# Optimization experiments

Measured on AMD Instinct MI355X. Metric: run time of the kernel, lower is better.

## Reference

```python
import jax, jax.numpy as jnp
import numpy as np

B, N, F_IN, H, C = 64, 512, 128, 128, 10
RATIO, NEG_SLOPE, LAMB = 0.5, 0.2, 1.0
K1 = int(np.ceil(RATIO * N))    # 256 nodes kept after pool1
K2 = int(np.ceil(RATIO * K1))   # 128 nodes kept after pool2


def _gcn(x, adj, W, b):
    # PyG-style GCN: add remaining self loops (fill=1, existing self-loop
    # weights kept), symmetric normalization, aggregate, add bias.
    h = x @ W
    n = adj.shape[-1]
    eye = jnp.eye(n, dtype=adj.dtype)
    diag = jnp.diagonal(adj, axis1=1, axis2=2)
    diag = jnp.where(diag == 0, 1.0, diag)
    a = adj * (1.0 - eye) + diag[:, :, None] * eye
    deg = a.sum(-1)
    dinv = jnp.where(deg > 0, 1.0 / jnp.sqrt(deg), 0.0)
    a_n = dinv[:, :, None] * a * dinv[:, None, :]
    return a_n @ h + b


def _info_score(x, adj):
    # NodeInformationScore: self loops added with weight 0, so
    # out = x - D^{-1/2} A D^{-1/2} x ; score = sum |out| over features.
    deg = adj.sum(-1)
    dinv = jnp.where(deg > 0, 1.0 / jnp.sqrt(deg), 0.0)
    a_n = dinv[:, :, None] * adj * dinv[:, None, :]
    return jnp.abs(x - a_n @ x).sum(-1)


def _sparsemax(z, mask):
    # Row-wise sparsemax over masked entries (each row has >=1 valid entry
    # thanks to the self loop). Shift by row max (sparsemax is shift-invariant).
    n = z.shape[-1]
    big_neg = jnp.asarray(-1e30, z.dtype)
    zmax = jnp.max(jnp.where(mask, z, big_neg), axis=-1, keepdims=True)
    zc = z - zmax
    zs = jnp.where(mask, zc, big_neg)
    zsort = -jnp.sort(-zs, axis=-1)                    # descending
    kk = jnp.arange(1, n + 1, dtype=z.dtype)
    cum = jnp.cumsum(zsort, axis=-1)
    cond = (1.0 + kk * zsort) > cum
    rho = jnp.sum(cond, axis=-1, keepdims=True)        # support size >= 1
    cum_rho = jnp.take_along_axis(cum, rho - 1, axis=-1)
    tau = (cum_rho - 1.0) / rho.astype(z.dtype)
    return jnp.maximum(zc - tau, 0.0) * mask


def _pool(x, adj, att, k):
    # HGPSLPool (sample=True, sparse=True, sl=True, lamb=1.0).
    score = _info_score(x, adj)
    _, perm = jax.lax.top_k(score, k)                  # [B, k] top nodes per graph
    xp = jnp.take_along_axis(x, perm[:, :, None], axis=1)
    # k_hop=3 neighborhood augmentation (two TwoHopNeighborhood passes);
    # augmented-only edges get attr 0, original edges keep their weight.
    s = jax.lax.stop_gradient((adj > 0).astype(x.dtype))
    for _ in range(2):
        s = jnp.where(s + s @ s > 0, 1.0, 0.0)

    def sub(m):
        m = jnp.take_along_axis(m, perm[:, :, None], axis=1)
        return jnp.take_along_axis(m, perm[:, None, :], axis=2)

    sp = sub(s)
    ap = sub(adj)                                      # kept-edge attrs
    eye = jnp.eye(k, dtype=x.dtype)
    sp = jnp.maximum(sp, eye)                          # add remaining self loops (attr fill 0)
    mask = sp > 0
    hh = att.shape[0] // 2
    a_i = xp @ att[:hh]                                # [B, k]
    a_j = xp @ att[hh:]
    logits = jax.nn.leaky_relu(a_i[:, :, None] + a_j[:, None, :], NEG_SLOPE) + LAMB * ap
    new_adj = _sparsemax(logits, mask)                 # learned sparse row-stochastic adjacency
    return xp, new_adj


def _readout(h):
    # torch_geometric gmp / gap concatenated (all graphs have equal node count)
    return jnp.concatenate([h.max(axis=1), h.mean(axis=1)], axis=-1)


def _forward(x, adj, W1, b1, att1, W2, b2, att2, W3, b3, Wl1, bl1, Wl2, bl2, Wl3, bl3):
    h = jax.nn.relu(_gcn(x, adj, W1, b1))
    h, adj1 = _pool(h, adj, att1, K1)
    x1 = _readout(h)
    h = jax.nn.relu(_gcn(h, adj1, W2, b2))
    h, adj2 = _pool(h, adj1, att2, K2)
    x2 = _readout(h)
    h = jax.nn.relu(_gcn(h, adj2, W3, b3))
    x3 = _readout(h)
    z = jax.nn.relu(x1) + jax.nn.relu(x2) + jax.nn.relu(x3)
    z = jax.nn.relu(z @ Wl1 + bl1)
    z = jax.nn.relu(z @ Wl2 + bl2)
    return jax.nn.log_softmax(z @ Wl3 + bl3, axis=-1)


def setup_inputs() -> dict:
    key = jax.random.key(0)
    ks = jax.random.split(key, 10)
    r = jax.random.uniform(ks[0], (B, N, N))
    up = jnp.triu((r < 10.0 / N).astype(jnp.float32), k=1)
    adj = up + jnp.swapaxes(up, 1, 2)   # symmetric binary adj, no self loops, avg degree ~10
    x = jax.random.normal(ks[1], (B, N, F_IN), dtype=jnp.float32)

    def lin(k, fi, fo):
        return jax.random.normal(k, (fi, fo), dtype=jnp.float32) / np.sqrt(fi)

    return {
        "x": x, "adj": adj,
        "W1": lin(ks[2], F_IN, H), "b1": jnp.zeros((H,), jnp.float32),
        "att1": jax.random.normal(ks[3], (2 * H,), jnp.float32) * 0.1,
        "W2": lin(ks[4], H, H), "b2": jnp.zeros((H,), jnp.float32),
        "att2": jax.random.normal(ks[5], (2 * H,), jnp.float32) * 0.1,
        "W3": lin(ks[6], H, H), "b3": jnp.zeros((H,), jnp.float32),
        "Wl1": lin(ks[7], 2 * H, H), "bl1": jnp.zeros((H,), jnp.float32),
        "Wl2": lin(ks[8], H, H // 2), "bl2": jnp.zeros((H // 2,), jnp.float32),
        "Wl3": lin(ks[9], H // 2, C), "bl3": jnp.zeros((C,), jnp.float32),
    }


def reference(x, adj, W1, b1, att1, W2, b2, att2, W3, b3, Wl1, bl1, Wl2, bl2, Wl3, bl3):
    return _forward(x, adj, W1, b1, att1, W2, b2, att2, W3, b3,
                    Wl1, bl1, Wl2, bl2, Wl3, bl3)
```

## Files before the change

### kernel.cpp

```cpp
#include <hip/hip_runtime.h>
#include <math.h>

#define BB 64
#define N1 512
#define K1 256
#define K2 128
#define HF 128
#define NC 10

__global__ __launch_bounds__(64) void deg_bits_kernel(const float* __restrict__ adj,
                                                      float* __restrict__ deg_gcn,
                                                      float* __restrict__ deg_info,
                                                      unsigned* __restrict__ bits, int n) {
    int row = blockIdx.x;
    int i = row % n;
    const float* ar = adj + (size_t)row * n;
    int lane = threadIdx.x;
    int W = n >> 5;
    unsigned* wrow = bits + (size_t)row * W;
    float s = 0.f;
    int kn = n >> 6;
    for (int k = 0; k < kn; k++) {
        float a = ar[k * 64 + lane];
        s += a;
        unsigned long long m = __ballot(a > 0.f);
        if (lane == 0) {
            wrow[2 * k]     = (unsigned)(m & 0xffffffffull);
            wrow[2 * k + 1] = (unsigned)(m >> 32);
        }
    }
    for (int off = 32; off > 0; off >>= 1) s += __shfl_down(s, off);
    if (lane == 0) {
        float diag = ar[i];
        deg_info[row] = s;
        deg_gcn[row]  = s + (diag == 0.f ? 1.f : 0.f);
    }
}

__global__ __launch_bounds__(128) void gemm128(const float* __restrict__ X,
                                               const float* __restrict__ W,
                                               float* __restrict__ Y, int M) {
    __shared__ float xl[16 * 128];
    int f = threadIdx.x;
    int r0 = blockIdx.x * 16;
    for (int idx = f; idx < 16 * 128; idx += 128) {
        int r = idx >> 7, k = idx & 127;
        xl[idx] = X[(size_t)(r0 + r) * 128 + k];
    }
    __syncthreads();
    float acc[16];
#pragma unroll
    for (int r = 0; r < 16; r++) acc[r] = 0.f;
    for (int k = 0; k < 128; k++) {
        float w = W[k * 128 + f];
#pragma unroll
        for (int r = 0; r < 16; r++) acc[r] += xl[r * 128 + k] * w;
    }
#pragma unroll
    for (int r = 0; r < 16; r++) Y[(size_t)(r0 + r) * 128 + f] = acc[r];
}

__global__ __launch_bounds__(128) void gcn_agg(const float* __restrict__ adj,
                                               const unsigned* __restrict__ bits,
                                               const float* __restrict__ deg_gcn,
                                               const float* __restrict__ hin,
                                               const float* __restrict__ bias,
                                               float* __restrict__ hout, int n) {
    __shared__ int idxl[512];
    __shared__ float coef[512];
    __shared__ int s_nnz;
    int row = blockIdx.x;
    int b = row / n, i = row % n;
    int tid = threadIdx.x;
    int W = n >> 5;
    const float* ar = adj + (size_t)row * n;
    const float* degb = deg_gcn + b * n;
    if (tid < 64) {
        int lane = tid;
        unsigned w = 0;
        if (lane < W) {
            w = bits[(size_t)row * W + lane];
            if ((i >> 5) == lane) w |= (1u << (i & 31));
        }
        int pc = __popc(w);
        int sc = pc;
#pragma unroll
        for (int off = 1; off < 64; off <<= 1) {
            int t = __shfl_up(sc, off);
            if (lane >= off) sc += t;
        }
        if (lane == 63) s_nnz = sc;
        int o = sc - pc;
        unsigned mm = w;
        while (mm) {
            int bp = __ffs(mm) - 1;
            mm &= mm - 1;
            int j = (lane << 5) + bp;
            float a = ar[j];
            if (j == i && a == 0.f) a = 1.f;
            float d = degb[j];
            float dj = d > 0.f ? 1.f / sqrtf(d) : 0.f;
            idxl[o] = j;
            coef[o] = a * dj;
            o++;
        }
    }
    __syncthreads();
    int nnz = s_nnz;
    int f = tid;
    const float* hb = hin + (size_t)b * n * HF;
    float acc = 0.f;
    int it = 0;
    for (; it + 4 <= nnz; it += 4) {
        int j0 = idxl[it], j1 = idxl[it + 1], j2 = idxl[it + 2], j3 = idxl[it + 3];
        float v0 = hb[(size_t)j0 * HF + f];
        float v1 = hb[(size_t)j1 * HF + f];
        float v2 = hb[(size_t)j2 * HF + f];
        float v3 = hb[(size_t)j3 * HF + f];
        float c0 = coef[it], c1 = coef[it + 1], c2 = coef[it + 2], c3 = coef[it + 3];
        acc += c0 * v0; acc += c1 * v1; acc += c2 * v2; acc += c3 * v3;
    }
    for (; it < nnz; it++) {
        acc += coef[it] * hb[(size_t)idxl[it] * HF + f];
    }
    float di_ = degb[i];
    float di = di_ > 0.f ? 1.f / sqrtf(di_) : 0.f;
    float v = di * acc + bias[f];
    hout[(size_t)row * HF + f] = fmaxf(v, 0.f);
}

__global__ __launch_bounds__(128) void info_score(const float* __restrict__ adj,
                                                  const unsigned* __restrict__ bits,
                                                  const float* __restrict__ deg_info,
                                                  const float* __restrict__ h,
                                                  float* __restrict__ score, int n) {
    __shared__ int idxl[512];
    __shared__ float coef[512];
    __shared__ int s_nnz;
    __shared__ float red[128];
    int row = blockIdx.x;
    int b = row / n, i = row % n;
    int tid = threadIdx.x;
    int W = n >> 5;
    const float* ar = adj + (size_t)row * n;
    const float* degb = deg_info + b * n;
    if (tid < 64) {
        int lane = tid;
        unsigned w = (lane < W) ? bits[(size_t)row * W + lane] : 0u;
        int pc = __popc(w);
        int sc = pc;
#pragma unroll
        for (int off = 1; off < 64; off <<= 1) {
            int t = __shfl_up(sc, off);
            if (lane >= off) sc += t;
        }
        if (lane == 63) s_nnz = sc;
        int o = sc - pc;
        unsigned mm = w;
        while (mm) {
            int bp = __ffs(mm) - 1;
            mm &= mm - 1;
            int j = (lane << 5) + bp;
            float a = ar[j];
            float d = degb[j];
            float dj = d > 0.f ? 1.f / sqrtf(d) : 0.f;
            idxl[o] = j;
            coef[o] = a * dj;
            o++;
        }
    }
    __syncthreads();
    int nnz = s_nnz;
    int f = tid;
    const float* hb = h + (size_t)b * n * HF;
    float acc = 0.f;
    int it = 0;
    for (; it + 4 <= nnz; it += 4) {
        int j0 = idxl[it], j1 = idxl[it + 1], j2 = idxl[it + 2], j3 = idxl[it + 3];
        float v0 = hb[(size_t)j0 * HF + f];
        float v1 = hb[(size_t)j1 * HF + f];
        float v2 = hb[(size_t)j2 * HF + f];
        float v3 = hb[(size_t)j3 * HF + f];
        float c0 = coef[it], c1 = coef[it + 1], c2 = coef[it + 2], c3 = coef[it + 3];
        acc += c0 * v0; acc += c1 * v1; acc += c2 * v2; acc += c3 * v3;
    }
    for (; it < nnz; it++) {
        acc += coef[it] * hb[(size_t)idxl[it] * HF + f];
    }
    float di_ = degb[i];
    float di = di_ > 0.f ? 1.f / sqrtf(di_) : 0.f;
    float diff = fabsf(hb[(size_t)i * HF + f] - di * acc);
    red[f] = diff;
    __syncthreads();
    for (int s = 64; s > 0; s >>= 1) {
        if (f < s) red[f] += red[f + s];
        __syncthreads();
    }
    if (f == 0) score[row] = red[0];
}

template <int NN>
__global__ __launch_bounds__(NN) void topk_kernel(const float* __restrict__ score,
                                                  int* __restrict__ perm, int k) {
    __shared__ unsigned long long keys[NN];
    int b = blockIdx.x, t = threadIdx.x;
    unsigned u = __float_as_uint(score[b * NN + t]);
    unsigned asc = (u & 0x80000000u) ? ~u : (u | 0x80000000u);
    unsigned desc = ~asc;
    keys[t] = ((unsigned long long)desc << 32) | (unsigned)t;
    __syncthreads();
    for (int kk = 2; kk <= NN; kk <<= 1) {
        for (int j = kk >> 1; j > 0; j >>= 1) {
            int ixj = t ^ j;
            if (ixj > t) {
                bool up = ((t & kk) == 0);
                unsigned long long a = keys[t], c = keys[ixj];
                if ((a > c) == up) { keys[t] = c; keys[ixj] = a; }
            }
            __syncthreads();
        }
    }
    if (t < k) perm[b * k + t] = (int)(keys[t] & 0xffffffffu);
}

__global__ __launch_bounds__(128) void gather_rows(const float* __restrict__ h,
                                                   const int* __restrict__ perm,
                                                   float* __restrict__ xp, int n, int k) {
    int idx = blockIdx.x;
    int b = idx / k;
    int f = threadIdx.x;
    int pi = perm[idx];
    xp[(size_t)idx * HF + f] = h[((size_t)b * n + pi) * HF + f];
}

__global__ __launch_bounds__(64) void bits_expand(const unsigned* __restrict__ sin,
                                                  unsigned* __restrict__ sout, int n, int W) {
    __shared__ unsigned rowi[16];
    __shared__ unsigned res[64];
    int row = blockIdx.x;
    int b = row / n;
    int t = threadIdx.x;
    if (t < W) rowi[t] = sin[(size_t)row * W + t];
    __syncthreads();
    int JC = 64 / W;
    int chunk = t / W, w = t % W;
    int wpc = W / JC;
    unsigned r = 0;
    const unsigned* sb = sin + (size_t)b * n * W;
    for (int wi = chunk * wpc; wi < (chunk + 1) * wpc; wi++) {
        unsigned m = rowi[wi];
        while (m) {
            int bpos = __ffs(m) - 1;
            m &= m - 1;
            int j = (wi << 5) + bpos;
            r |= sb[(size_t)j * W + w];
        }
    }
    res[t] = r;
    __syncthreads();
    if (t < W) {
        unsigned acc = rowi[t];
        for (int c = 0; c < JC; c++) acc |= res[c * W + t];
        sout[(size_t)row * W + t] = acc;
    }
}

__global__ __launch_bounds__(128) void attn_dots(const float* __restrict__ xp,
                                                 const float* __restrict__ att,
                                                 float* __restrict__ ai, float* __restrict__ aj) {
    __shared__ float red[128];
    int idx = blockIdx.x;
    int f = threadIdx.x;
    float v = xp[(size_t)idx * HF + f];
    red[f] = v * att[f];
    __syncthreads();
    for (int s = 64; s > 0; s >>= 1) {
        if (f < s) red[f] += red[f + s];
        __syncthreads();
    }
    if (f == 0) ai[idx] = red[0];
    __syncthreads();
    red[f] = v * att[128 + f];
    __syncthreads();
    for (int s = 64; s > 0; s >>= 1) {
        if (f < s) red[f] += red[f + s];
        __syncthreads();
    }
    if (f == 0) aj[idx] = red[0];
}

template <int K>
__global__ __launch_bounds__(256) void sparsemax_wave(const float* __restrict__ ai,
                                                      const float* __restrict__ aj,
                                                      const int* __restrict__ perm,
                                                      const float* __restrict__ adjprev,
                                                      const unsigned* __restrict__ s4,
                                                      float* __restrict__ newadj,
                                                      int nprev, int Wprev) {
    constexpr int EPL = K / 64;
    int lane = threadIdx.x & 63;
    int wid = threadIdx.x >> 6;
    int r = blockIdx.x * 4 + wid;
    int b = r / K, i = r % K;
    int pi = perm[r];
    float air = ai[r];
    const float* aprow = adjprev + ((size_t)b * nprev + pi) * nprev;
    const unsigned* srow = s4 + ((size_t)b * nprev + pi) * Wprev;
    const int* permb = perm + b * K;
    const float* ajb = aj + b * K;

    float z[EPL], zc[EPL], zs[EPL];
    unsigned mbits = 0;
    float m = -1e30f;
#pragma unroll
    for (int e = 0; e < EPL; e++) {
        int j = lane * EPL + e;
        int pj = permb[j];
        float ap = aprow[pj];
        unsigned wb = srow[pj >> 5];
        bool mask = ((wb >> (pj & 31)) & 1u) || (i == j);
        float v = air + ajb[j];
        float lr = v > 0.f ? v : 0.2f * v;
        z[e] = lr + ap;
        if (mask) mbits |= (1u << e);
        m = fmaxf(m, mask ? z[e] : -1e30f);
    }
#pragma unroll
    for (int off = 1; off < 64; off <<= 1) m = fmaxf(m, __shfl_xor(m, off));

#pragma unroll
    for (int e = 0; e < EPL; e++) {
        zc[e] = z[e] - m;
        zs[e] = ((mbits >> e) & 1u) ? zc[e] : -1e30f;
    }

    for (int kk = 2; kk <= K; kk <<= 1) {
        for (int d = kk >> 1; d >= EPL; d >>= 1) {
            int lm = d / EPL;
#pragma unroll
            for (int e = 0; e < EPL; e++) {
                float other = __shfl_xor(zs[e], lm);
                int idx = lane * EPL + e;
                bool desc = (idx & kk) == 0;
                bool lower = (lane & lm) == 0;
                zs[e] = (desc == lower) ? fmaxf(zs[e], other) : fminf(zs[e], other);
            }
        }
#pragma unroll
        for (int dd = EPL >> 1; dd >= 1; dd >>= 1) {
            if (kk > dd) {
#pragma unroll
                for (int e = 0; e < EPL; e++) {
                    if (!(e & dd)) {
                        int ep = e | dd;
                        int idx = lane * EPL + e;
                        bool desc = (idx & kk) == 0;
                        float a = zs[e], c = zs[ep];
                        float mx = fmaxf(a, c), mn = fminf(a, c);
                        zs[e] = desc ? mx : mn;
                        zs[ep] = desc ? mn : mx;
                    }
                }
            }
        }
    }

    float c[EPL];
    c[0] = zs[0];
#pragma unroll
    for (int e = 1; e < EPL; e++) c[e] = c[e - 1] + zs[e];
    float lsum = c[EPL - 1];
    float sc = lsum;
#pragma unroll
    for (int off = 1; off < 64; off <<= 1) {
        float t = __shfl_up(sc, off);
        if (lane >= off) sc += t;
    }
    float excl = sc - lsum;
#pragma unroll
    for (int e = 0; e < EPL; e++) c[e] += excl;

    int cnt = 0;
#pragma unroll
    for (int e = 0; e < EPL; e++) {
        int idx = lane * EPL + e;
        if (1.f + (float)(idx + 1) * zs[e] > c[e]) cnt++;
    }
#pragma unroll
    for (int off = 1; off < 64; off <<= 1) cnt += __shfl_xor(cnt, off);
    int rho = cnt;

    int pos = rho - 1;
    int tl = pos / EPL, te = pos % EPL;
    float g[EPL];
#pragma unroll
    for (int e = 0; e < EPL; e++) g[e] = __shfl(c[e], tl);
    float cum_rho = g[0];
#pragma unroll
    for (int e = 1; e < EPL; e++) cum_rho = (te == e) ? g[e] : cum_rho;
    float tau = (cum_rho - 1.f) / (float)rho;

    float o[EPL];
#pragma unroll
    for (int e = 0; e < EPL; e++)
        o[e] = fmaxf(zc[e] - tau, 0.f) * (((mbits >> e) & 1u) ? 1.f : 0.f);

    float* orow = newadj + (size_t)r * K + lane * EPL;
    if constexpr (EPL == 4) {
        *reinterpret_cast<float4*>(orow) = make_float4(o[0], o[1], o[2], o[3]);
    } else {
        *reinterpret_cast<float2*>(orow) = make_float2(o[0], o[1]);
    }
}

__global__ __launch_bounds__(128) void readout_partial(const float* __restrict__ h,
                                                       float* __restrict__ pmax,
                                                       float* __restrict__ psum,
                                                       int n, int nch) {
    int blk = blockIdx.x;
    int c = blk % nch;
    int f = threadIdx.x;
    const float* hb = h + ((size_t)(blk / nch) * n + c * 32) * HF;
    float mx = -INFINITY, sm = 0.f;
#pragma unroll
    for (int i = 0; i < 32; i++) {
        float v = hb[(size_t)i * HF + f];
        mx = fmaxf(mx, v);
        sm += v;
    }
    pmax[(size_t)blk * HF + f] = mx;
    psum[(size_t)blk * HF + f] = sm;
}

__global__ __launch_bounds__(128) void readout_combine(const float* __restrict__ pmax,
                                                       const float* __restrict__ psum,
                                                       float* __restrict__ out,
                                                       int n, int nch) {
    int b = blockIdx.x;
    int f = threadIdx.x;
    float mx = -INFINITY, sm = 0.f;
    for (int c = 0; c < nch; c++) {
        mx = fmaxf(mx, pmax[((size_t)b * nch + c) * HF + f]);
        sm += psum[((size_t)b * nch + c) * HF + f];
    }
    out[b * 256 + f] = mx;
    out[b * 256 + 128 + f] = sm / (float)n;
}

__global__ __launch_bounds__(256) void mlp_kernel(const float* __restrict__ x1,
                                                  const float* __restrict__ x2,
                                                  const float* __restrict__ x3,
                                                  const float* __restrict__ Wl1,
                                                  const float* __restrict__ bl1,
                                                  const float* __restrict__ Wl2,
                                                  const float* __restrict__ bl2,
                                                  const float* __restrict__ Wl3,
                                                  const float* __restrict__ bl3,
                                                  float* __restrict__ out) {
    __shared__ float z[256];
    __shared__ float h1[128];
    __shared__ float h2[64];
    __shared__ float o[NC];
    int b = blockIdx.x;
    int t = threadIdx.x;
    z[t] = fmaxf(x1[b * 256 + t], 0.f) + fmaxf(x2[b * 256 + t], 0.f) + fmaxf(x3[b * 256 + t], 0.f);
    __syncthreads();
    if (t < 128) {
        float acc = bl1[t];
        for (int k = 0; k < 256; k++) acc += z[k] * Wl1[k * 128 + t];
        h1[t] = fmaxf(acc, 0.f);
    }
    __syncthreads();
    if (t < 64) {
        float acc = bl2[t];
        for (int k = 0; k < 128; k++) acc += h1[k] * Wl2[k * 64 + t];
        h2[t] = fmaxf(acc, 0.f);
    }
    __syncthreads();
    if (t < NC) {
        float acc = bl3[t];
        for (int k = 0; k < 64; k++) acc += h2[k] * Wl3[k * NC + t];
        o[t] = acc;
    }
    __syncthreads();
    if (t == 0) {
        float mx = o[0];
        for (int c = 1; c < NC; c++) mx = fmaxf(mx, o[c]);
        float s = 0.f;
        for (int c = 0; c < NC; c++) s += expf(o[c] - mx);
        float lse = mx + logf(s);
        for (int c = 0; c < NC; c++) out[b * NC + c] = o[c] - lse;
    }
}

extern "C" void kernel_launch(void* const* d_in, const int* in_sizes, int n_in,
                              void* d_out, int out_size, void* d_ws, size_t ws_size,
                              hipStream_t stream) {
    const float* x    = (const float*)d_in[0];
    const float* adj  = (const float*)d_in[1];
    const float* W1   = (const float*)d_in[2];
    const float* b1   = (const float*)d_in[3];
    const float* att1 = (const float*)d_in[4];
    const float* W2   = (const float*)d_in[5];
    const float* b2   = (const float*)d_in[6];
    const float* att2 = (const float*)d_in[7];
    const float* W3   = (const float*)d_in[8];
    const float* b3   = (const float*)d_in[9];
    const float* Wl1  = (const float*)d_in[10];
    const float* bl1  = (const float*)d_in[11];
    const float* Wl2  = (const float*)d_in[12];
    const float* bl2  = (const float*)d_in[13];
    const float* Wl3  = (const float*)d_in[14];
    const float* bl3  = (const float*)d_in[15];
    float* out = (float*)d_out;

    char* wp = (char*)d_ws;
    auto allocf = [&](size_t n) { float* r = (float*)wp; wp += n * sizeof(float); return r; };
    auto alloci = [&](size_t n) { int* r = (int*)wp; wp += n * sizeof(int); return r; };
    auto allocu = [&](size_t n) { unsigned* r = (unsigned*)wp; wp += n * sizeof(unsigned); return r; };

    float* deg_gcn1  = allocf(BB * N1);
    float* deg_info1 = allocf(BB * N1);
    float* hw        = allocf((size_t)BB * N1 * HF);
    float* h1        = allocf((size_t)BB * N1 * HF);
    float* score1    = allocf(BB * N1);
    int*   perm1     = alloci(BB * K1);
    float* xp1       = allocf((size_t)BB * K1 * HF);
    unsigned* bitsA  = allocu((size_t)BB * N1 * 16);
    unsigned* bitsB  = allocu((size_t)BB * N1 * 16);
    float* ai1       = allocf(BB * K1);
    float* aj1       = allocf(BB * K1);
    float* adj1      = allocf((size_t)BB * K1 * K1);
    float* x1r       = allocf(BB * 256);
    float* deg_gcn2  = allocf(BB * K1);
    float* deg_info2 = allocf(BB * K1);
    float* h2        = allocf((size_t)BB * K1 * HF);
    float* score2    = allocf(BB * K1);
    int*   perm2     = alloci(BB * K2);
    float* xp2       = allocf((size_t)BB * K2 * HF);
    float* ai2       = allocf(BB * K2);
    float* aj2       = allocf(BB * K2);
    float* adj2      = allocf((size_t)BB * K2 * K2);
    float* x2r       = allocf(BB * 256);
    float* deg_gcn3  = allocf(BB * K2);
    float* deg_info3 = allocf(BB * K2);
    float* h3        = allocf((size_t)BB * K2 * HF);
    float* x3r       = allocf(BB * 256);
    float* pmax      = allocf((size_t)BB * 8 * HF);
    float* psum      = allocf((size_t)BB * 8 * HF);

    deg_bits_kernel<<<dim3(BB * N1), dim3(64), 0, stream>>>(adj, deg_gcn1, deg_info1, bitsA, N1);
    gemm128<<<dim3(BB * N1 / 16), dim3(128), 0, stream>>>(x, W1, hw, BB * N1);
    gcn_agg<<<dim3(BB * N1), dim3(128), 0, stream>>>(adj, bitsA, deg_gcn1, hw, b1, h1, N1);
    info_score<<<dim3(BB * N1), dim3(128), 0, stream>>>(adj, bitsA, deg_info1, h1, score1, N1);
    topk_kernel<512><<<dim3(BB), dim3(512), 0, stream>>>(score1, perm1, K1);
    gather_rows<<<dim3(BB * K1), dim3(128), 0, stream>>>(h1, perm1, xp1, N1, K1);
    bits_expand<<<dim3(BB * N1), dim3(64), 0, stream>>>(bitsA, bitsB, N1, 16);
    bits_expand<<<dim3(BB * N1), dim3(64), 0, stream>>>(bitsB, bitsA, N1, 16);
    attn_dots<<<dim3(BB * K1), dim3(128), 0, stream>>>(xp1, att1, ai1, aj1);
    sparsemax_wave<K1><<<dim3(BB * K1 / 4), dim3(256), 0, stream>>>(ai1, aj1, perm1, adj, bitsA, adj1, N1, 16);
    readout_partial<<<dim3(BB * (K1 / 32)), dim3(128), 0, stream>>>(xp1, pmax, psum, K1, K1 / 32);
    readout_combine<<<dim3(BB), dim3(128), 0, stream>>>(pmax, psum, x1r, K1, K1 / 32);

    deg_bits_kernel<<<dim3(BB * K1), dim3(64), 0, stream>>>(adj1, deg_gcn2, deg_info2, bitsA, K1);
    gemm128<<<dim3(BB * K1 / 16), dim3(128), 0, stream>>>(xp1, W2, hw, BB * K1);
    gcn_agg<<<dim3(BB * K1), dim3(128), 0, stream>>>(adj1, bitsA, deg_gcn2, hw, b2, h2, K1);
    info_score<<<dim3(BB * K1), dim3(128), 0, stream>>>(adj1, bitsA, deg_info2, h2, score2, K1);
    topk_kernel<256><<<dim3(BB), dim3(256), 0, stream>>>(score2, perm2, K2);
    gather_rows<<<dim3(BB * K2), dim3(128), 0, stream>>>(h2, perm2, xp2, K1, K2);
    bits_expand<<<dim3(BB * K1), dim3(64), 0, stream>>>(bitsA, bitsB, K1, 8);
    bits_expand<<<dim3(BB * K1), dim3(64), 0, stream>>>(bitsB, bitsA, K1, 8);
    attn_dots<<<dim3(BB * K2), dim3(128), 0, stream>>>(xp2, att2, ai2, aj2);
    sparsemax_wave<K2><<<dim3(BB * K2 / 4), dim3(256), 0, stream>>>(ai2, aj2, perm2, adj1, bitsA, adj2, K1, 8);
    readout_partial<<<dim3(BB * (K2 / 32)), dim3(128), 0, stream>>>(xp2, pmax, psum, K2, K2 / 32);
    readout_combine<<<dim3(BB), dim3(128), 0, stream>>>(pmax, psum, x2r, K2, K2 / 32);

    deg_bits_kernel<<<dim3(BB * K2), dim3(64), 0, stream>>>(adj2, deg_gcn3, deg_info3, bitsB, K2);
    gemm128<<<dim3(BB * K2 / 16), dim3(128), 0, stream>>>(xp2, W3, hw, BB * K2);
    gcn_agg<<<dim3(BB * K2), dim3(128), 0, stream>>>(adj2, bitsB, deg_gcn3, hw, b3, h3, K2);
    readout_partial<<<dim3(BB * (K2 / 32)), dim3(128), 0, stream>>>(h3, pmax, psum, K2, K2 / 32);
    readout_combine<<<dim3(BB), dim3(128), 0, stream>>>(pmax, psum, x3r, K2, K2 / 32);

    mlp_kernel<<<dim3(BB), dim3(256), 0, stream>>>(x1r, x2r, x3r, Wl1, bl1, Wl2, bl2, Wl3, bl3, out);
}
```

Measured before the change: 540.6 us.

## Compact neighbor lists and expand only kept rows in second hop pass

The bitset neighborhood expansion now first builds a compact shared-memory list of set-bit column indices using a wave prefix sum. Each lane then gathers neighbor words from that list with four loads in flight, instead of walking bitmask words serially per chunk. The second expansion pass is replaced by a perm-aware variant that computes only the k kept rows, which cuts that pass's blocks in half. Sparsemax now indexes the compacted bitset by output row. This adds a 2KB shared list per block and a scan step per block.

```diff
diff --git a/kernel.cpp b/kernel.cpp
--- a/kernel.cpp
+++ b/kernel.cpp
@@ -236,32 +236,106 @@
 __global__ __launch_bounds__(64) void bits_expand(const unsigned* __restrict__ sin,
                                                   unsigned* __restrict__ sout, int n, int W) {
     __shared__ unsigned rowi[16];
+    __shared__ int jlist[512];
     __shared__ unsigned res[64];
+    __shared__ int s_nnz;
     int row = blockIdx.x;
     int b = row / n;
     int t = threadIdx.x;
-    if (t < W) rowi[t] = sin[(size_t)row * W + t];
-    __syncthreads();
+    unsigned w = (t < W) ? sin[(size_t)row * W + t] : 0u;
+    if (t < W) rowi[t] = w;
+    int pc = __popc(w);
+    int sc = pc;
+#pragma unroll
+    for (int off = 1; off < 64; off <<= 1) {
+        int v = __shfl_up(sc, off);
+        if (t >= off) sc += v;
+    }
+    if (t == 63) s_nnz = sc;
+    int o = sc - pc;
+    unsigned mm = w;
+    while (mm) {
+        int bp = __ffs(mm) - 1;
+        mm &= mm - 1;
+        jlist[o++] = (t << 5) + bp;
+    }
+    __syncthreads();
+    int nnz = s_nnz;
     int JC = 64 / W;
-    int chunk = t / W, w = t % W;
-    int wpc = W / JC;
+    int chunk = t / W, wi = t % W;
+    const unsigned* sb = sin + (size_t)b * n * W;
     unsigned r = 0;
-    const unsigned* sb = sin + (size_t)b * n * W;
-    for (int wi = chunk * wpc; wi < (chunk + 1) * wpc; wi++) {
-        unsigned m = rowi[wi];
-        while (m) {
-            int bpos = __ffs(m) - 1;
-            m &= m - 1;
-            int j = (wi << 5) + bpos;
-            r |= sb[(size_t)j * W + w];
-        }
-    }
+    int q = chunk;
+    for (; q + 3 * JC < nnz; q += 4 * JC) {
+        int j0 = jlist[q], j1 = jlist[q + JC], j2 = jlist[q + 2 * JC], j3 = jlist[q + 3 * JC];
+        unsigned v0 = sb[(size_t)j0 * W + wi];
+        unsigned v1 = sb[(size_t)j1 * W + wi];
+        unsigned v2 = sb[(size_t)j2 * W + wi];
+        unsigned v3 = sb[(size_t)j3 * W + wi];
+        r |= v0 | v1 | v2 | v3;
+    }
+    for (; q < nnz; q += JC) r |= sb[(size_t)jlist[q] * W + wi];
     res[t] = r;
     __syncthreads();
     if (t < W) {
         unsigned acc = rowi[t];
         for (int c = 0; c < JC; c++) acc |= res[c * W + t];
         sout[(size_t)row * W + t] = acc;
+    }
+}
+
+__global__ __launch_bounds__(64) void bits_expand_perm(const unsigned* __restrict__ sin,
+                                                       const int* __restrict__ perm,
+                                                       unsigned* __restrict__ sout,
+                                                       int n, int W, int k) {
+    __shared__ unsigned rowi[16];
+    __shared__ int jlist[512];
+    __shared__ unsigned res[64];
+    __shared__ int s_nnz;
+    int r0 = blockIdx.x;
+    int b = r0 / k;
+    int pi = perm[r0];
+    int t = threadIdx.x;
+    size_t srow = (size_t)(b * n + pi) * W;
+    unsigned w = (t < W) ? sin[srow + t] : 0u;
+    if (t < W) rowi[t] = w;
+    int pc = __popc(w);
+    int sc = pc;
+#pragma unroll
+    for (int off = 1; off < 64; off <<= 1) {
+        int v = __shfl_up(sc, off);
+        if (t >= off) sc += v;
+    }
+    if (t == 63) s_nnz = sc;
+    int o = sc - pc;
+    unsigned mm = w;
+    while (mm) {
+        int bp = __ffs(mm) - 1;
+        mm &= mm - 1;
+        jlist[o++] = (t << 5) + bp;
+    }
+    __syncthreads();
+    int nnz = s_nnz;
+    int JC = 64 / W;
+    int chunk = t / W, wi = t % W;
+    const unsigned* sb = sin + (size_t)b * n * W;
+    unsigned r = 0;
+    int q = chunk;
+    for (; q + 3 * JC < nnz; q += 4 * JC) {
+        int j0 = jlist[q], j1 = jlist[q + JC], j2 = jlist[q + 2 * JC], j3 = jlist[q + 3 * JC];
+        unsigned v0 = sb[(size_t)j0 * W + wi];
+        unsigned v1 = sb[(size_t)j1 * W + wi];
+        unsigned v2 = sb[(size_t)j2 * W + wi];
+        unsigned v3 = sb[(size_t)j3 * W + wi];
+        r |= v0 | v1 | v2 | v3;
+    }
+    for (; q < nnz; q += JC) r |= sb[(size_t)jlist[q] * W + wi];
+    res[t] = r;
+    __syncthreads();
+    if (t < W) {
+        unsigned acc = rowi[t];
+        for (int c = 0; c < JC; c++) acc |= res[c * W + t];
+        sout[(size_t)r0 * W + t] = acc;
     }
 }
 
@@ -294,7 +368,7 @@
                                                       const float* __restrict__ aj,
                                                       const int* __restrict__ perm,
                                                       const float* __restrict__ adjprev,
-                                                      const unsigned* __restrict__ s4,
+                                                      const unsigned* __restrict__ s4c,
                                                       float* __restrict__ newadj,
                                                       int nprev, int Wprev) {
     constexpr int EPL = K / 64;
@@ -305,7 +379,7 @@
     int pi = perm[r];
     float air = ai[r];
     const float* aprow = adjprev + ((size_t)b * nprev + pi) * nprev;
-    const unsigned* srow = s4 + ((size_t)b * nprev + pi) * Wprev;
+    const unsigned* srow = s4c + (size_t)r * Wprev;
     const int* permb = perm + b * K;
     const float* ajb = aj + b * K;
 
@@ -556,7 +630,7 @@
     topk_kernel<512><<<dim3(BB), dim3(512), 0, stream>>>(score1, perm1, K1);
     gather_rows<<<dim3(BB * K1), dim3(128), 0, stream>>>(h1, perm1, xp1, N1, K1);
     bits_expand<<<dim3(BB * N1), dim3(64), 0, stream>>>(bitsA, bitsB, N1, 16);
-    bits_expand<<<dim3(BB * N1), dim3(64), 0, stream>>>(bitsB, bitsA, N1, 16);
+    bits_expand_perm<<<dim3(BB * K1), dim3(64), 0, stream>>>(bitsB, perm1, bitsA, N1, 16, K1);
     attn_dots<<<dim3(BB * K1), dim3(128), 0, stream>>>(xp1, att1, ai1, aj1);
     sparsemax_wave<K1><<<dim3(BB * K1 / 4), dim3(256), 0, stream>>>(ai1, aj1, perm1, adj, bitsA, adj1, N1, 16);
     readout_partial<<<dim3(BB * (K1 / 32)), dim3(128), 0, stream>>>(xp1, pmax, psum, K1, K1 / 32);
@@ -569,7 +643,7 @@
     topk_kernel<256><<<dim3(BB), dim3(256), 0, stream>>>(score2, perm2, K2);
     gather_rows<<<dim3(BB * K2), dim3(128), 0, stream>>>(h2, perm2, xp2, K1, K2);
     bits_expand<<<dim3(BB * K1), dim3(64), 0, stream>>>(bitsA, bitsB, K1, 8);
-    bits_expand<<<dim3(BB * K1), dim3(64), 0, stream>>>(bitsB, bitsA, K1, 8);
+    bits_expand_perm<<<dim3(BB * K2), dim3(64), 0, stream>>>(bitsB, perm2, bitsA, K1, 8, K2);
     attn_dots<<<dim3(BB * K2), dim3(128), 0, stream>>>(xp2, att2, ai2, aj2);
     sparsemax_wave<K2><<<dim3(BB * K2 / 4), dim3(256), 0, stream>>>(ai2, aj2, perm2, adj1, bitsA, adj2, K1, 8);
     readout_partial<<<dim3(BB * (K2 / 32)), dim3(128), 0, stream>>>(xp2, pmax, psum, K2, K2 / 32);
```

Measured after the change: 508.7 us. 5.9% less time.
